# Kernel tuning notes

Hardware: AMD Instinct MI355X
Metric: run time of the kernel (lower is better)

## Reference

```python
import jax, jax.numpy as jnp
import numpy as np

B, S, D, H = 2, 2048, 1024, 16
HD = D // H               # head_dim = input_size / num_heads
STEPS = 1                 # update_steps_max extra Hopfield update steps
LN_EPS = 1e-5
SCALING = 1.0 / np.sqrt(HD)  # beta = 1/sqrt(head_dim)


def layernorm(x, g, b):
    m = x.mean(-1, keepdims=True)
    v = ((x - m) ** 2).mean(-1, keepdims=True)
    return (x - m) * jax.lax.rsqrt(v + LN_EPS) * g + b


def setup_inputs() -> dict:
    key = jax.random.key(0)
    ks = jax.random.split(key, 9)
    s = 0.02
    f32 = jnp.float32
    return {
        "data": jax.random.normal(ks[0], (B, S, D), f32),
        # affine LayerNorm params (stored / state / projection patterns)
        "g_k": jnp.ones((D,), f32), "b_k": jnp.zeros((D,), f32),
        "g_q": jnp.ones((D,), f32), "b_q": jnp.zeros((D,), f32),
        "g_v": jnp.ones((D,), f32), "b_v": jnp.zeros((D,), f32),
        # in-projections (q/k/v) and out-projection of HopfieldCore
        "Wq": jax.random.normal(ks[1], (D, D), f32) * s, "bq": jnp.zeros((D,), f32),
        "Wk": jax.random.normal(ks[2], (D, D), f32) * s, "bk": jnp.zeros((D,), f32),
        "Wv": jax.random.normal(ks[3], (D, D), f32) * s, "bv": jnp.zeros((D,), f32),
        "Wo": jax.random.normal(ks[4], (D, D), f32) * s, "bo": jnp.zeros((D,), f32),
    }


def reference(data, g_k, b_k, g_q, b_q, g_v, b_v,
              Wq, bq, Wk, bk, Wv, bv, Wo, bo):
    # single input tensor used as stored / state / projection pattern
    xk = layernorm(data, g_k, b_k)   # stored pattern  -> keys
    xq = layernorm(data, g_q, b_q)   # state pattern   -> queries
    xv = layernorm(data, g_v, b_v)   # pattern proj    -> values

    split = lambda t: t.reshape(B, S, H, HD).transpose(0, 2, 1, 3)  # [B,H,S,HD]
    q = split(xq @ Wq + bq)
    k = split(xk @ Wk + bk)
    v = split(xv @ Wv + bv)

    def assoc(q):  # xi = softmax(beta * q K^T)
        return jax.nn.softmax(
            jnp.einsum('bhqd,bhkd->bhqk', q, k) * SCALING, axis=-1)

    xi = assoc(q)
    for _ in range(STEPS):           # iterative Hopfield update: q <- xi K
        q = jnp.einsum('bhqk,bhkd->bhqd', xi, k)
        xi = assoc(q)

    out = jnp.einsum('bhqk,bhkd->bhqd', xi, v)        # retrieve with values
    out = out.transpose(0, 2, 1, 3).reshape(B, S, D)  # merge heads
    return out @ Wo + bo
```

## Files before the change

kernel.cpp:

```cpp
#include <hip/hip_runtime.h>
#include <hip/hip_bf16.h>

#define B_  2
#define S_  2048
#define D_  1024
#define H_  16
#define HD_ 64
#define M_  4096


typedef __attribute__((ext_vector_type(8))) short short8;
typedef __attribute__((ext_vector_type(4))) float f32x4;

#define CE_ 0.1803368801111204f
#define SD_ 56

typedef __attribute__((address_space(1))) const unsigned GU;
typedef __attribute__((address_space(3))) unsigned LU;
static __device__ __forceinline__ void glds16(const void* g, void* l){
  __builtin_amdgcn_global_load_lds((GU*)g, (LU*)l, 16, 0, 0);
}

static __device__ __forceinline__ unsigned short f2bfc(float f){
  union{float f; unsigned u;} c; c.f = f;
  return (unsigned short)((c.u + 0x8000u) >> 16);
}
static __device__ __forceinline__ unsigned pk2bf(float a, float b){
  union{float f; unsigned u;} ca, cb; ca.f=a; cb.f=b;
  return __builtin_amdgcn_perm(cb.u + 0x8000u, ca.u + 0x8000u, 0x07060302u);
}
static __device__ __forceinline__ unsigned pk2bft(float a, float b){
  union{float f; unsigned u;} ca, cb; ca.f=a; cb.f=b;
  return __builtin_amdgcn_perm(cb.u, ca.u, 0x07060302u);
}

__global__ __launch_bounds__(256) void prep_kernel(
  const float* __restrict__ data, float* __restrict__ mean, float* __restrict__ rstd,
  const float* __restrict__ Wq, const float* __restrict__ Wk,
  const float* __restrict__ Wv, const float* __restrict__ Wo,
  const float* __restrict__ gq, const float* __restrict__ gk, const float* __restrict__ gv,
  const float* __restrict__ blq, const float* __restrict__ blk, const float* __restrict__ blv,
  const float* __restrict__ bpq, const float* __restrict__ bpk, const float* __restrict__ bpv,
  unsigned short* __restrict__ WT, float* __restrict__ bf)
{
  __shared__ unsigned short tile[64][72];
  __shared__ float red[4][64];
  int bid = blockIdx.x, t = threadIdx.x;
  if (bid < 1024){
    int row = bid*4 + (t>>6);
    int l = t & 63;
    const float4* xr = (const float4*)(data + (size_t)row*D_);
    float s = 0.f, ss = 0.f;
    #pragma unroll
    for (int i=0;i<4;i++){
      float4 v = xr[l + 64*i];
      s  += v.x+v.y+v.z+v.w;
      ss += v.x*v.x+v.y*v.y+v.z*v.z+v.w*v.w;
    }
    #pragma unroll
    for (int m=1;m<64;m<<=1){ s += __shfl_xor(s, m, 64); ss += __shfl_xor(ss, m, 64); }
    if (l==0){
      float me = s*(1.0f/D_);
      float var = ss*(1.0f/D_) - me*me;
      mean[row] = me;
      rstd[row] = rsqrtf(var + 1e-5f);
    }
  } else if (bid < 2048){
    int idx = bid - 1024;
    int z = idx >> 8, rem = idx & 255;
    int k0 = (rem>>4)*64, n0 = (rem&15)*64;
    const float* W = (z==0)?Wq:(z==1)?Wk:(z==2)?Wv:Wo;
    const float* g = (z==0)?gq:(z==1)?gk:(z==2)?gv:(const float*)0;
    unsigned short* out = WT + ((size_t)z<<20);
    {
      int kr = t>>2, c16 = (t&3)*16;
      float gs = g ? g[k0+kr]*((z==0)?CE_:1.0f) : 1.0f;
      const float* src = W + (size_t)(k0+kr)*D_ + n0 + c16;
      float4 w0 = *(const float4*)(src);
      float4 w1 = *(const float4*)(src+4);
      float4 w2 = *(const float4*)(src+8);
      float4 w3 = *(const float4*)(src+12);
      unsigned* tp = (unsigned*)&tile[kr][c16];
      tp[0]=pk2bf(w0.x*gs,w0.y*gs); tp[1]=pk2bf(w0.z*gs,w0.w*gs);
      tp[2]=pk2bf(w1.x*gs,w1.y*gs); tp[3]=pk2bf(w1.z*gs,w1.w*gs);
      tp[4]=pk2bf(w2.x*gs,w2.y*gs); tp[5]=pk2bf(w2.z*gs,w2.w*gs);
      tp[6]=pk2bf(w3.x*gs,w3.y*gs); tp[7]=pk2bf(w3.z*gs,w3.w*gs);
    }
    __syncthreads();
    {
      int nr = t>>2, kc = (t&3)*16;
      union { uint4 v[2]; unsigned short u[16]; } st;
      #pragma unroll
      for (int i=0;i<16;i++) st.u[i] = tile[kc+i][nr];
      unsigned short* dst = out + (size_t)(n0+nr)*D_ + k0 + kc;
      *(uint4*)(dst)     = st.v[0];
      *(uint4*)(dst + 8) = st.v[1];
    }
  } else {
    int idx = bid - 2048;
    int z = idx >> 4, xb = idx & 15;
    const float* W  = (z==0)?Wq:(z==1)?Wk:Wv;
    const float* bl = (z==0)?blq:(z==1)?blk:blv;
    const float* bp = (z==0)?bpq:(z==1)?bpk:bpv;
    int nl = t & 63, kg = t >> 6;
    int n = xb*64 + nl;
    float acc = 0.f;
    for (int k = kg*256; k < (kg+1)*256; k++)
      acc += bl[k] * W[(size_t)k*D_ + n];
    red[kg][nl] = acc;
    __syncthreads();
    if (t < 64){
      int nn = xb*64 + t;
      float v = red[0][t]+red[1][t]+red[2][t]+red[3][t] + bp[nn];
      bf[z*D_ + nn] = (z==0) ? v*CE_ : v;
    }
  }
}

__global__ __launch_bounds__(256) void gemm_qkv(
  const float* __restrict__ data,
  const unsigned short* __restrict__ WT,
  const float* __restrict__ biasf,
  const float* __restrict__ mean, const float* __restrict__ rstd,
  unsigned short* __restrict__ qv, unsigned short* __restrict__ kb,
  unsigned short* __restrict__ kT, unsigned short* __restrict__ vT)
{
  int z = blockIdx.z;
  const unsigned short* Bt = WT + ((size_t)z<<20);
  const float* bias = biasf + z*D_;
  unsigned short* oN = (z==0)?qv:(z==1)?kb:(unsigned short*)0;
  unsigned short* oT = (z==0)?(unsigned short*)0:(z==1)?kT:vT;

  __shared__ __align__(16) unsigned short As[128*SD_];
  __shared__ __align__(16) unsigned short Bs[128*32];
  int tid = threadIdx.x, w = tid>>6, l = tid&63;
  int m0 = blockIdx.x*128, n0 = blockIdx.y*128;
  int wr = (w>>1)*64, wc = (w&1)*64;
  int lr = l&15, qd = l>>4;
  int srow = tid>>2, scol = (tid&3)*8;

  float rs0 = rstd[m0+srow],    nm0 = -mean[m0+srow]*rs0;
  float rs1 = rstd[m0+srow+64], nm1 = -mean[m0+srow+64]*rs1;

  const unsigned short* gB = Bt + (size_t)(n0 + w*32 + (l>>2))*D_ + (l&3)*8;
  unsigned short* lB0 = &Bs[(w*32)*32];
  unsigned short* lB1 = &Bs[(w*32+16)*32];

  const f32x4 fz = {0.f,0.f,0.f,0.f};
  f32x4 acc[4][4];
  #pragma unroll
  for (int i=0;i<4;i++)
    #pragma unroll
    for (int j=0;j<4;j++) acc[i][j] = fz;

  for (int kk=0; kk<D_; kk+=32){
    __syncthreads();
    glds16(gB + kk,                 lB0);
    glds16(gB + kk + (size_t)16*D_, lB1);
    {
      const float* p0 = data + (size_t)(m0+srow   )*D_ + kk + scol;
      const float* p1 = data + (size_t)(m0+srow+64)*D_ + kk + scol;
      float4 a0 = *(const float4*)(p0), a0b = *(const float4*)(p0+4);
      float4 a1 = *(const float4*)(p1), a1b = *(const float4*)(p1+4);
      uint4 o0, o1;
      o0.x = pk2bf(fmaf(a0.x ,rs0,nm0), fmaf(a0.y ,rs0,nm0));
      o0.y = pk2bf(fmaf(a0.z ,rs0,nm0), fmaf(a0.w ,rs0,nm0));
      o0.z = pk2bf(fmaf(a0b.x,rs0,nm0), fmaf(a0b.y,rs0,nm0));
      o0.w = pk2bf(fmaf(a0b.z,rs0,nm0), fmaf(a0b.w,rs0,nm0));
      o1.x = pk2bf(fmaf(a1.x ,rs1,nm1), fmaf(a1.y ,rs1,nm1));
      o1.y = pk2bf(fmaf(a1.z ,rs1,nm1), fmaf(a1.w ,rs1,nm1));
      o1.z = pk2bf(fmaf(a1b.x,rs1,nm1), fmaf(a1b.y,rs1,nm1));
      o1.w = pk2bf(fmaf(a1b.z,rs1,nm1), fmaf(a1b.w,rs1,nm1));
      *(uint4*)(As + srow*SD_      + scol) = o0;
      *(uint4*)(As + (srow+64)*SD_ + scol) = o1;
    }
    __syncthreads();
    short8 af[4], bfr[4];
    #pragma unroll
    for (int i=0;i<4;i++) af[i]  = *(const short8*)(As + (wr + i*16 + lr)*SD_ + qd*8);
    #pragma unroll
    for (int j=0;j<4;j++) bfr[j] = *(const short8*)(Bs + (wc + j*16 + lr)*32 + qd*8);
    #pragma unroll
    for (int i=0;i<4;i++)
      #pragma unroll
      for (int j=0;j<4;j++)
        acc[i][j] = __builtin_amdgcn_mfma_f32_16x16x32_bf16(af[i], bfr[j], acc[i][j], 0, 0, 0);
  }

  #pragma unroll
  for (int j=0;j<4;j++){
    int n = n0 + wc + j*16 + lr;
    float bias_n = bias[n];
    #pragma unroll
    for (int i=0;i<4;i++){
      int mb = m0 + wr + i*16 + qd*4;
      float v0 = acc[i][j][0] + bias_n;
      float v1 = acc[i][j][1] + bias_n;
      float v2 = acc[i][j][2] + bias_n;
      float v3 = acc[i][j][3] + bias_n;
      if (oN){
        oN[(size_t)(mb+0)*D_ + n] = f2bfc(v0);
        oN[(size_t)(mb+1)*D_ + n] = f2bfc(v1);
        oN[(size_t)(mb+2)*D_ + n] = f2bfc(v2);
        oN[(size_t)(mb+3)*D_ + n] = f2bfc(v3);
      }
      if (oT){
        int bb = mb >> 11, sI = mb & (S_-1);
        int hh = n >> 6,  dd = n & 63;
        uint2 pk; pk.x = pk2bf(v0, v1); pk.y = pk2bf(v2, v3);
        *(uint2*)(oT + (size_t)((bb*H_ + hh)*HD_ + dd)*S_ + sI) = pk;
      }
    }
  }
}

__global__ __launch_bounds__(256) void gemm_out(
  const unsigned short* __restrict__ A,
  const unsigned short* __restrict__ Bt,
  const float* __restrict__ bo,
  float* __restrict__ Cf)
{
  __shared__ __align__(16) unsigned short As[128*32];
  __shared__ __align__(16) unsigned short Bs[128*32];
  int tid = threadIdx.x, w = tid>>6, l = tid&63;
  int m0 = blockIdx.x*128, n0 = blockIdx.y*128;
  int wr = (w>>1)*64, wc = (w&1)*64;
  int lr = l&15, qd = l>>4;

  const unsigned short* gA = A  + (size_t)(m0 + w*32 + (l>>2))*D_ + (l&3)*8;
  const unsigned short* gB = Bt + (size_t)(n0 + w*32 + (l>>2))*D_ + (l&3)*8;
  unsigned short* lA0 = &As[(w*32)*32];
  unsigned short* lA1 = &As[(w*32+16)*32];
  unsigned short* lB0 = &Bs[(w*32)*32];
  unsigned short* lB1 = &Bs[(w*32+16)*32];

  const f32x4 fz = {0.f,0.f,0.f,0.f};
  f32x4 acc[4][4];
  #pragma unroll
  for (int i=0;i<4;i++)
    #pragma unroll
    for (int j=0;j<4;j++) acc[i][j] = fz;

  for (int kk=0; kk<D_; kk+=32){
    __syncthreads();
    glds16(gA + kk,                 lA0);
    glds16(gA + kk + (size_t)16*D_, lA1);
    glds16(gB + kk,                 lB0);
    glds16(gB + kk + (size_t)16*D_, lB1);
    __syncthreads();
    short8 af[4], bfr[4];
    #pragma unroll
    for (int i=0;i<4;i++) af[i]  = *(const short8*)(As + (wr + i*16 + lr)*32 + qd*8);
    #pragma unroll
    for (int j=0;j<4;j++) bfr[j] = *(const short8*)(Bs + (wc + j*16 + lr)*32 + qd*8);
    #pragma unroll
    for (int i=0;i<4;i++)
      #pragma unroll
      for (int j=0;j<4;j++)
        acc[i][j] = __builtin_amdgcn_mfma_f32_16x16x32_bf16(af[i], bfr[j], acc[i][j], 0, 0, 0);
  }

  #pragma unroll
  for (int j=0;j<4;j++){
    int n = n0 + wc + j*16 + lr;
    float bias_n = bo[n];
    #pragma unroll
    for (int i=0;i<4;i++){
      int mb = m0 + wr + i*16 + qd*4;
      Cf[(size_t)(mb+0)*D_ + n] = acc[i][j][0] + bias_n;
      Cf[(size_t)(mb+1)*D_ + n] = acc[i][j][1] + bias_n;
      Cf[(size_t)(mb+2)*D_ + n] = acc[i][j][2] + bias_n;
      Cf[(size_t)(mb+3)*D_ + n] = acc[i][j][3] + bias_n;
    }
  }
}

__global__ __launch_bounds__(256) void attn_fused(
  unsigned short* __restrict__ QO,
  const unsigned short* __restrict__ K,
  const unsigned short* __restrict__ KT,
  const unsigned short* __restrict__ VT)
{
  int qt = blockIdx.x;
  int h  = blockIdx.y;
  int b  = qt >> 4;
  int bh = b*H_ + h;
  int tid = threadIdx.x, w = tid>>6, l = tid&63;
  int lr = l&15, qd = l>>4;
  int r8 = tid>>3, c8 = (tid&7)*8;
  int chf = c8>>5, co = c8&31;

  __shared__ __align__(16) unsigned short sK[2][64*SD_];
  __shared__ __align__(16) unsigned short sV[2][64*SD_];
  __shared__ __align__(16) unsigned short sP[4][2][16*SD_];

  const f32x4 fz = {0.f,0.f,0.f,0.f};

  unsigned short* Qbase = QO + (size_t)(qt*128 + w*32) * D_ + h*64;
  short8 qf[2][2];
  #pragma unroll
  for (int gg=0; gg<2; gg++)
    #pragma unroll
    for (int hf=0; hf<2; hf++)
      qf[gg][hf] = *(const short8*)(Qbase + (size_t)(gg*16+lr)*D_ + hf*32 + qd*8);

  const unsigned short* Khead = K + (size_t)(b*S_)*D_ + h*64;
  const unsigned short* Vh0 = KT + (size_t)bh*HD_*S_;
  const unsigned short* Vh1 = VT + (size_t)bh*HD_*S_;
  unsigned short* Pw0 = &sP[w][0][0];
  unsigned short* Pw1 = &sP[w][1][0];

  f32x4 oacc[2][4];
  float lac[2];

  uint4 kr0, kr1, vr0, vr1;
  {
    kr0 = *(const uint4*)(Khead + (size_t)(r8   )*D_ + c8);
    kr1 = *(const uint4*)(Khead + (size_t)(r8+32)*D_ + c8);
    vr0 = *(const uint4*)(Vh0 + (size_t)(r8   )*S_ + c8);
    vr1 = *(const uint4*)(Vh0 + (size_t)(r8+32)*S_ + c8);
  }

  #pragma unroll 1
  for (int phase=0; phase<2; phase++){
    const unsigned short* Vhead = phase ? Vh1 : Vh0;
    lac[0]=0.f; lac[1]=0.f;
    #pragma unroll
    for (int gg=0;gg<2;gg++)
      #pragma unroll
      for (int t=0;t<4;t++) oacc[gg][t]=fz;

    for (int kt=0; kt<S_; kt+=64){
      __syncthreads();
      *(uint4*)(&sK[chf][(r8   )*SD_ + co]) = kr0;
      *(uint4*)(&sK[chf][(r8+32)*SD_ + co]) = kr1;
      *(uint4*)(&sV[chf][(r8   )*SD_ + co]) = vr0;
      *(uint4*)(&sV[chf][(r8+32)*SD_ + co]) = vr1;
      __syncthreads();

      {
        int nkt = kt + 64;
        const unsigned short* Vn = Vhead;
        if (nkt >= S_){ nkt = 0; Vn = Vh1; }
        kr0 = *(const uint4*)(Khead + (size_t)(nkt+r8   )*D_ + c8);
        kr1 = *(const uint4*)(Khead + (size_t)(nkt+r8+32)*D_ + c8);
        vr0 = *(const uint4*)(Vn + (size_t)(r8   )*S_ + nkt + c8);
        vr1 = *(const uint4*)(Vn + (size_t)(r8+32)*S_ + nkt + c8);
      }

      f32x4 sc[2][4];
      #pragma unroll
      for (int st=0; st<4; st++){
        short8 kA0 = *(const short8*)(&sK[0][(st*16+lr)*SD_ + qd*8]);
        short8 kA1 = *(const short8*)(&sK[1][(st*16+lr)*SD_ + qd*8]);
        #pragma unroll
        for (int gg=0; gg<2; gg++){
          f32x4 z = fz;
          z = __builtin_amdgcn_mfma_f32_16x16x32_bf16(kA0, qf[gg][0], z, 0,0,0);
          z = __builtin_amdgcn_mfma_f32_16x16x32_bf16(kA1, qf[gg][1], z, 0,0,0);
          sc[gg][st] = z;
        }
      }
      short8 pf[2][2];
      #pragma unroll
      for (int gg=0; gg<2; gg++){
        #pragma unroll
        for (int st=0; st<4; st++){
          float p0=__builtin_amdgcn_exp2f(sc[gg][st][0]);
          float p1=__builtin_amdgcn_exp2f(sc[gg][st][1]);
          float p2=__builtin_amdgcn_exp2f(sc[gg][st][2]);
          float p3=__builtin_amdgcn_exp2f(sc[gg][st][3]);
          lac[gg] += (p0+p1)+(p2+p3);
          uint2 pk; pk.x = pk2bft(p0,p1); pk.y = pk2bft(p2,p3);
          unsigned short* Ph = (st&2) ? Pw1 : Pw0;
          *(uint2*)(Ph + lr*SD_ + (st&1)*16 + qd*4) = pk;
        }
        pf[gg][0] = *(const short8*)(Pw0 + lr*SD_ + qd*8);
        pf[gg][1] = *(const short8*)(Pw1 + lr*SD_ + qd*8);
      }
      #pragma unroll
      for (int dt=0; dt<4; dt++){
        short8 vA0 = *(const short8*)(&sV[0][(dt*16+lr)*SD_ + qd*8]);
        short8 vA1 = *(const short8*)(&sV[1][(dt*16+lr)*SD_ + qd*8]);
        #pragma unroll
        for (int gg=0; gg<2; gg++){
          oacc[gg][dt] = __builtin_amdgcn_mfma_f32_16x16x32_bf16(vA0, pf[gg][0], oacc[gg][dt], 0,0,0);
          oacc[gg][dt] = __builtin_amdgcn_mfma_f32_16x16x32_bf16(vA1, pf[gg][1], oacc[gg][dt], 0,0,0);
        }
      }
    }

    #pragma unroll
    for (int gg=0;gg<2;gg++){
      lac[gg] += __shfl_xor(lac[gg], 16, 64);
      lac[gg] += __shfl_xor(lac[gg], 32, 64);
    }

    if (phase==0){
      #pragma unroll
      for (int gg=0;gg<2;gg++){
        float iv = CE_ * __builtin_amdgcn_rcpf(lac[gg]);
        #pragma unroll
        for (int dt=0;dt<4;dt++){
          uint2 pk;
          pk.x = pk2bf(oacc[gg][dt][0]*iv, oacc[gg][dt][1]*iv);
          pk.y = pk2bf(oacc[gg][dt][2]*iv, oacc[gg][dt][3]*iv);
          unsigned short* Ph = (dt&2) ? Pw1 : Pw0;
          *(uint2*)(Ph + lr*SD_ + (dt&1)*16 + qd*4) = pk;
        }
        qf[gg][0] = *(const short8*)(Pw0 + lr*SD_ + qd*8);
        qf[gg][1] = *(const short8*)(Pw1 + lr*SD_ + qd*8);
      }
    } else {
      #pragma unroll
      for (int gg=0;gg<2;gg++){
        float iv = __builtin_amdgcn_rcpf(lac[gg]);
        unsigned short* Ob = QO + (size_t)(qt*128 + w*32 + gg*16 + lr)*D_ + h*64;
        #pragma unroll
        for (int dt=0;dt<4;dt++){
          uint2 pk;
          pk.x = pk2bf(oacc[gg][dt][0]*iv, oacc[gg][dt][1]*iv);
          pk.y = pk2bf(oacc[gg][dt][2]*iv, oacc[gg][dt][3]*iv);
          *(uint2*)(Ob + dt*16 + qd*4) = pk;
        }
      }
    }
  }
}

extern "C" void kernel_launch(void* const* d_in, const int* in_sizes, int n_in,
                              void* d_out, int out_size, void* d_ws, size_t ws_size,
                              hipStream_t stream){
  const float* data = (const float*)d_in[0];
  const float* g_k  = (const float*)d_in[1];
  const float* b_k  = (const float*)d_in[2];
  const float* g_q  = (const float*)d_in[3];
  const float* b_q  = (const float*)d_in[4];
  const float* g_v  = (const float*)d_in[5];
  const float* b_v  = (const float*)d_in[6];
  const float* Wq   = (const float*)d_in[7];
  const float* bq   = (const float*)d_in[8];
  const float* Wk   = (const float*)d_in[9];
  const float* bk   = (const float*)d_in[10];
  const float* Wv   = (const float*)d_in[11];
  const float* bv   = (const float*)d_in[12];
  const float* Wo   = (const float*)d_in[13];
  const float* bo   = (const float*)d_in[14];
  float* out = (float*)d_out;

  char* ws = (char*)d_ws;
  const size_t MB = (size_t)1<<20;
  unsigned short* q    = (unsigned short*)(ws);
  unsigned short* kb   = (unsigned short*)(ws + 8*MB);
  unsigned short* WT   = (unsigned short*)(ws + 16*MB);
  unsigned short* WTo  = WT + ((size_t)3<<20);
  float*          bfld = (float*)(ws + 24*MB);
  float*          mean = bfld + 3*D_;
  float*          rstd = mean + M_;
  unsigned short* vT   = (unsigned short*)d_out;
  unsigned short* kT   = (unsigned short*)((char*)d_out + 8*MB);

  dim3 gb(256);
  prep_kernel<<<dim3(2096), gb, 0, stream>>>(data, mean, rstd,
                                             Wq, Wk, Wv, Wo, g_q, g_k, g_v,
                                             b_q, b_k, b_v, bq, bk, bv, WT, bfld);
  gemm_qkv<<<dim3(32,8,3), gb, 0, stream>>>(data, WT, bfld, mean, rstd, q, kb, kT, vT);
  attn_fused<<<dim3(32, H_), gb, 0, stream>>>(q, kb, kT, vT);
  gemm_out<<<dim3(32,8), gb, 0, stream>>>(q, WTo, bo, out);
}
```

Measured before the change: 277.4 us.

## Materialize normalized bf16 activations in prep, load them via async LDS copies

```diff
diff --git a/kernel.cpp b/kernel.cpp
--- a/kernel.cpp
+++ b/kernel.cpp
@@ -35,39 +35,20 @@
 }
 
 __global__ __launch_bounds__(256) void prep_kernel(
-  const float* __restrict__ data, float* __restrict__ mean, float* __restrict__ rstd,
+  const float* __restrict__ data,
   const float* __restrict__ Wq, const float* __restrict__ Wk,
   const float* __restrict__ Wv, const float* __restrict__ Wo,
   const float* __restrict__ gq, const float* __restrict__ gk, const float* __restrict__ gv,
   const float* __restrict__ blq, const float* __restrict__ blk, const float* __restrict__ blv,
   const float* __restrict__ bpq, const float* __restrict__ bpk, const float* __restrict__ bpv,
-  unsigned short* __restrict__ WT, float* __restrict__ bf)
+  unsigned short* __restrict__ WT, unsigned short* __restrict__ xhat,
+  float* __restrict__ bf)
 {
   __shared__ unsigned short tile[64][72];
   __shared__ float red[4][64];
   int bid = blockIdx.x, t = threadIdx.x;
   if (bid < 1024){
-    int row = bid*4 + (t>>6);
-    int l = t & 63;
-    const float4* xr = (const float4*)(data + (size_t)row*D_);
-    float s = 0.f, ss = 0.f;
-    #pragma unroll
-    for (int i=0;i<4;i++){
-      float4 v = xr[l + 64*i];
-      s  += v.x+v.y+v.z+v.w;
-      ss += v.x*v.x+v.y*v.y+v.z*v.z+v.w*v.w;
-    }
-    #pragma unroll
-    for (int m=1;m<64;m<<=1){ s += __shfl_xor(s, m, 64); ss += __shfl_xor(ss, m, 64); }
-    if (l==0){
-      float me = s*(1.0f/D_);
-      float var = ss*(1.0f/D_) - me*me;
-      mean[row] = me;
-      rstd[row] = rsqrtf(var + 1e-5f);
-    }
-  } else if (bid < 2048){
-    int idx = bid - 1024;
-    int z = idx >> 8, rem = idx & 255;
+    int z = bid >> 8, rem = bid & 255;
     int k0 = (rem>>4)*64, n0 = (rem&15)*64;
     const float* W = (z==0)?Wq:(z==1)?Wk:(z==2)?Wv:Wo;
     const float* g = (z==0)?gq:(z==1)?gk:(z==2)?gv:(const float*)0;
@@ -96,6 +77,32 @@
       *(uint4*)(dst)     = st.v[0];
       *(uint4*)(dst + 8) = st.v[1];
     }
+  } else if (bid < 2048){
+    int row = (bid-1024)*4 + (t>>6);
+    int l = t & 63;
+    const float4* xr = (const float4*)(data + (size_t)row*D_);
+    float4 v[4];
+    float s = 0.f, ss = 0.f;
+    #pragma unroll
+    for (int i=0;i<4;i++){
+      v[i] = xr[l + 64*i];
+      s  += v[i].x+v[i].y+v[i].z+v[i].w;
+      ss += v[i].x*v[i].x+v[i].y*v[i].y+v[i].z*v[i].z+v[i].w*v[i].w;
+    }
+    #pragma unroll
+    for (int m=1;m<64;m<<=1){ s += __shfl_xor(s, m, 64); ss += __shfl_xor(ss, m, 64); }
+    float me = s*(1.0f/D_);
+    float var = ss*(1.0f/D_) - me*me;
+    float rs = rsqrtf(var + 1e-5f);
+    float nm = -me*rs;
+    unsigned short* xo = xhat + (size_t)row*D_;
+    #pragma unroll
+    for (int i=0;i<4;i++){
+      uint2 pk;
+      pk.x = pk2bf(fmaf(v[i].x,rs,nm), fmaf(v[i].y,rs,nm));
+      pk.y = pk2bf(fmaf(v[i].z,rs,nm), fmaf(v[i].w,rs,nm));
+      *(uint2*)(xo + 4*l + 256*i) = pk;
+    }
   } else {
     int idx = bid - 2048;
     int z = idx >> 4, xb = idx & 15;
@@ -118,10 +125,9 @@
 }
 
 __global__ __launch_bounds__(256) void gemm_qkv(
-  const float* __restrict__ data,
+  const unsigned short* __restrict__ xhat,
   const unsigned short* __restrict__ WT,
   const float* __restrict__ biasf,
-  const float* __restrict__ mean, const float* __restrict__ rstd,
   unsigned short* __restrict__ qv, unsigned short* __restrict__ kb,
   unsigned short* __restrict__ kT, unsigned short* __restrict__ vT)
 {
@@ -131,18 +137,17 @@
   unsigned short* oN = (z==0)?qv:(z==1)?kb:(unsigned short*)0;
   unsigned short* oT = (z==0)?(unsigned short*)0:(z==1)?kT:vT;
 
-  __shared__ __align__(16) unsigned short As[128*SD_];
+  __shared__ __align__(16) unsigned short As[128*32];
   __shared__ __align__(16) unsigned short Bs[128*32];
   int tid = threadIdx.x, w = tid>>6, l = tid&63;
   int m0 = blockIdx.x*128, n0 = blockIdx.y*128;
   int wr = (w>>1)*64, wc = (w&1)*64;
   int lr = l&15, qd = l>>4;
-  int srow = tid>>2, scol = (tid&3)*8;
-
-  float rs0 = rstd[m0+srow],    nm0 = -mean[m0+srow]*rs0;
-  float rs1 = rstd[m0+srow+64], nm1 = -mean[m0+srow+64]*rs1;
-
-  const unsigned short* gB = Bt + (size_t)(n0 + w*32 + (l>>2))*D_ + (l&3)*8;
+
+  const unsigned short* gA = xhat + (size_t)(m0 + w*32 + (l>>2))*D_ + (l&3)*8;
+  const unsigned short* gB = Bt   + (size_t)(n0 + w*32 + (l>>2))*D_ + (l&3)*8;
+  unsigned short* lA0 = &As[(w*32)*32];
+  unsigned short* lA1 = &As[(w*32+16)*32];
   unsigned short* lB0 = &Bs[(w*32)*32];
   unsigned short* lB1 = &Bs[(w*32+16)*32];
 
@@ -155,29 +160,14 @@
 
   for (int kk=0; kk<D_; kk+=32){
     __syncthreads();
+    glds16(gA + kk,                 lA0);
+    glds16(gA + kk + (size_t)16*D_, lA1);
     glds16(gB + kk,                 lB0);
     glds16(gB + kk + (size_t)16*D_, lB1);
-    {
-      const float* p0 = data + (size_t)(m0+srow   )*D_ + kk + scol;
-      const float* p1 = data + (size_t)(m0+srow+64)*D_ + kk + scol;
-      float4 a0 = *(const float4*)(p0), a0b = *(const float4*)(p0+4);
-      float4 a1 = *(const float4*)(p1), a1b = *(const float4*)(p1+4);
-      uint4 o0, o1;
-      o0.x = pk2bf(fmaf(a0.x ,rs0,nm0), fmaf(a0.y ,rs0,nm0));
-      o0.y = pk2bf(fmaf(a0.z ,rs0,nm0), fmaf(a0.w ,rs0,nm0));
-      o0.z = pk2bf(fmaf(a0b.x,rs0,nm0), fmaf(a0b.y,rs0,nm0));
-      o0.w = pk2bf(fmaf(a0b.z,rs0,nm0), fmaf(a0b.w,rs0,nm0));
-      o1.x = pk2bf(fmaf(a1.x ,rs1,nm1), fmaf(a1.y ,rs1,nm1));
-      o1.y = pk2bf(fmaf(a1.z ,rs1,nm1), fmaf(a1.w ,rs1,nm1));
-      o1.z = pk2bf(fmaf(a1b.x,rs1,nm1), fmaf(a1b.y,rs1,nm1));
-      o1.w = pk2bf(fmaf(a1b.z,rs1,nm1), fmaf(a1b.w,rs1,nm1));
-      *(uint4*)(As + srow*SD_      + scol) = o0;
-      *(uint4*)(As + (srow+64)*SD_ + scol) = o1;
-    }
     __syncthreads();
     short8 af[4], bfr[4];
     #pragma unroll
-    for (int i=0;i<4;i++) af[i]  = *(const short8*)(As + (wr + i*16 + lr)*SD_ + qd*8);
+    for (int i=0;i<4;i++) af[i]  = *(const short8*)(As + (wr + i*16 + lr)*32 + qd*8);
     #pragma unroll
     for (int j=0;j<4;j++) bfr[j] = *(const short8*)(Bs + (wc + j*16 + lr)*32 + qd*8);
     #pragma unroll
@@ -454,17 +444,17 @@
   unsigned short* kb   = (unsigned short*)(ws + 8*MB);
   unsigned short* WT   = (unsigned short*)(ws + 16*MB);
   unsigned short* WTo  = WT + ((size_t)3<<20);
-  float*          bfld = (float*)(ws + 24*MB);
-  float*          mean = bfld + 3*D_;
-  float*          rstd = mean + M_;
+  unsigned short* xhat = (unsigned short*)(ws + 24*MB);
+  float*          bfld = (float*)(ws + 32*MB);
   unsigned short* vT   = (unsigned short*)d_out;
   unsigned short* kT   = (unsigned short*)((char*)d_out + 8*MB);
 
   dim3 gb(256);
-  prep_kernel<<<dim3(2096), gb, 0, stream>>>(data, mean, rstd,
+  prep_kernel<<<dim3(2096), gb, 0, stream>>>(data,
                                              Wq, Wk, Wv, Wo, g_q, g_k, g_v,
-                                             b_q, b_k, b_v, bq, bk, bv, WT, bfld);
-  gemm_qkv<<<dim3(32,8,3), gb, 0, stream>>>(data, WT, bfld, mean, rstd, q, kb, kT, vT);
+                                             b_q, b_k, b_v, bq, bk, bv,
+                                             WT, xhat, bfld);
+  gemm_qkv<<<dim3(32,8,3), gb, 0, stream>>>(xhat, WT, bfld, q, kb, kT, vT);
   attn_fused<<<dim3(32, H_), gb, 0, stream>>>(q, kb, kT, vT);
   gemm_out<<<dim3(32,8), gb, 0, stream>>>(q, WTo, bo, out);
 }
```

Measured after the change: 266.8 us. -3.8%, faster.
